# Optimization experiments

Measured on AMD Instinct MI355X. Metric: run time of the kernel, lower is better.

## Reference

```python
import jax, jax.numpy as jnp
import numpy as np

N = 50000   # nodes
R = 3       # relations
E = 300000  # edges per relation
H, D = 4, 32  # heads, per-head dim (hidden_feat=128)
IN, HID, OUT = 128, 128, 64
SLOPE = 0.2  # DGL GATConv leaky_relu negative slope


def setup_inputs() -> dict:
    key = jax.random.key(0)
    ks = jax.random.split(key, 12)
    s = 0.05
    return {
        "x": jax.random.normal(ks[0], (N, IN), jnp.float32),
        "edges": jax.random.randint(ks[1], (R, 2, E), 0, N, jnp.int64),
        "W1": jax.random.normal(ks[2], (R, IN, H * D), jnp.float32) * s,
        "al1": jax.random.normal(ks[3], (R, H, D), jnp.float32) * s,
        "ar1": jax.random.normal(ks[4], (R, H, D), jnp.float32) * s,
        "b1": jnp.zeros((R, H, D), jnp.float32),
        "W2": jax.random.normal(ks[5], (R, HID, H * D), jnp.float32) * s,
        "al2": jax.random.normal(ks[6], (R, H, D), jnp.float32) * s,
        "ar2": jax.random.normal(ks[7], (R, H, D), jnp.float32) * s,
        "b2": jnp.zeros((R, H, D), jnp.float32),
        "Wl": jax.random.normal(ks[8], (HID, OUT), jnp.float32) * s,
        "bl": jnp.zeros((OUT,), jnp.float32),
    }


def rgat_layer(h, edges, W, al, ar, b):
    """HeteroGraphConv(sum) of per-relation GATConv. h: [N,F]. Returns [N,H,D]."""
    out = jnp.zeros((N, H, D), h.dtype)
    for r in range(R):  # small fixed relation count
        src, dst = edges[r, 0], edges[r, 1]
        feat = (h @ W[r]).reshape(N, H, D)                  # per-relation projection
        el = jnp.einsum("nhd,hd->nh", feat, al[r])          # [N,H]
        er = jnp.einsum("nhd,hd->nh", feat, ar[r])          # [N,H]
        e = jax.nn.leaky_relu(el[src] + er[dst], SLOPE)      # [E,H]
        # edge softmax over incoming edges per destination node
        emax = jax.ops.segment_max(e, dst, num_segments=N)   # [N,H]
        ex = jnp.exp(e - emax[dst])
        denom = jax.ops.segment_sum(ex, dst, num_segments=N) # [N,H]
        alpha = ex / denom[dst]                               # [E,H]
        msg = feat[src] * alpha[:, :, None]                   # [E,H,D]
        out = out + jax.ops.segment_sum(msg, dst, num_segments=N) + b[r]
    return out


def reference(x, edges, W1, al1, ar1, b1, W2, al2, ar2, b2, Wl, bl):
    h = rgat_layer(x, edges, W1, al1, ar1, b1).reshape(N, H * D)
    h = jax.nn.relu(h)  # dropout is identity in eval mode
    h = rgat_layer(h, edges, W2, al2, ar2, b2).reshape(N, H * D)
    return h @ Wl + bl  # [N, OUT]
```

## Files before the change

### kernel.cpp

```cpp
#include <hip/hip_runtime.h>
#include <hip/hip_bf16.h>
#include <hip/hip_fp16.h>
#include <type_traits>

#define Nn 50000
#define RR 3
#define EE 300000

typedef __attribute__((ext_vector_type(8))) short short8;
typedef __attribute__((ext_vector_type(4))) short short4v;
typedef __attribute__((ext_vector_type(4))) float floatx4;

__device__ __forceinline__ short f2bf(float f) {
    __hip_bfloat16 h = __float2bfloat16(f);
    return *reinterpret_cast<short*>(&h);
}


__global__ void count_wswz_kernel(const int* __restrict__ edges, int* __restrict__ counts,
                                  int* __restrict__ ord,
                                  const float* __restrict__ W1, const float* __restrict__ W2,
                                  short* __restrict__ Z) {
    int bx = blockIdx.x;
    if (bx >= 440) {
        int idx = (bx - 440) * 256 + threadIdx.x;
        if (idx >= 12288) return;
        int lane = idx & 63;
        int nt = (idx >> 6) & 7;
        int kt = (idx >> 9) & 3;
        int rl = idx >> 11;
        int layer = rl / 3, r = rl % 3;
        const float* W = (layer ? W2 : W1) + (size_t)r * 16384;
        int n = nt * 16 + (lane & 15);
        int k0 = kt * 32 + (lane >> 4) * 8;
        short8 v;
        #pragma unroll
        for (int j = 0; j < 8; ++j) v[j] = f2bf(W[(size_t)(k0 + j) * 128 + n]);
        *(short8*)&Z[(size_t)idx * 8] = v;
        return;
    }
    int i = bx * 256 + threadIdx.x;
    if (i >= RR * EE / 8) return;
    int g = i * 8;
    int r = g / EE, e0 = g - r * EE;
    const int* db = &edges[(size_t)r * 2 * EE + EE + e0];
    int4 d0 = *(const int4*)db;
    int4 d1 = *(const int4*)(db + 4);
    int* cb = counts + r * Nn;
    int4 o0, o1;
    o0.x = atomicAdd(&cb[d0.x], 1);
    o0.y = atomicAdd(&cb[d0.y], 1);
    o0.z = atomicAdd(&cb[d0.z], 1);
    o0.w = atomicAdd(&cb[d0.w], 1);
    o1.x = atomicAdd(&cb[d1.x], 1);
    o1.y = atomicAdd(&cb[d1.y], 1);
    o1.z = atomicAdd(&cb[d1.z], 1);
    o1.w = atomicAdd(&cb[d1.w], 1);
    *(int4*)&ord[g] = o0;
    *(int4*)&ord[g + 4] = o1;
}

__global__ __launch_bounds__(256) void alloc_kernel(const int* __restrict__ counts,
                                                    int* __restrict__ row_start,
                                                    int* __restrict__ totals) {
    __shared__ int s[256];
    __shared__ int base_s;
    int r = blockIdx.y;
    int tid = threadIdx.x;
    int n = blockIdx.x * 256 + tid;
    int idx = r * Nn + n;
    int c = (n < Nn) ? counts[idx] : 0;
    s[tid] = c;
    __syncthreads();
    #pragma unroll
    for (int off = 1; off < 256; off <<= 1) {
        int v = 0;
        if (tid >= off) v = s[tid - off];
        __syncthreads();
        if (tid >= off) s[tid] += v;
        __syncthreads();
    }
    if (tid == 255) base_s = atomicAdd(&totals[r], s[255]);
    __syncthreads();
    if (n < Nn) row_start[idx] = base_s + s[tid] - c;
}

__global__ void scatter_kernel(const int* __restrict__ edges, const int* __restrict__ ord,
                               const int* __restrict__ row_start, int2* __restrict__ csr) {
    int i = blockIdx.x * blockDim.x + threadIdx.x;
    if (i >= RR * EE / 8) return;
    int g = i * 8;
    int r = g / EE, e0 = g - r * EE;
    const int* sb = &edges[(size_t)r * 2 * EE + e0];
    const int* db = sb + EE;
    int4 s0 = *(const int4*)sb, s1 = *(const int4*)(sb + 4);
    int4 d0 = *(const int4*)db, d1 = *(const int4*)(db + 4);
    int4 o0 = *(const int4*)&ord[g], o1 = *(const int4*)&ord[g + 4];
    const int* rs = row_start + r * Nn;
    int2* cb = csr + (size_t)r * EE;
    cb[rs[d0.x] + o0.x] = make_int2(s0.x, d0.x);
    cb[rs[d0.y] + o0.y] = make_int2(s0.y, d0.y);
    cb[rs[d0.z] + o0.z] = make_int2(s0.z, d0.z);
    cb[rs[d0.w] + o0.w] = make_int2(s0.w, d0.w);
    cb[rs[d1.x] + o1.x] = make_int2(s1.x, d1.x);
    cb[rs[d1.y] + o1.y] = make_int2(s1.y, d1.y);
    cb[rs[d1.z] + o1.z] = make_int2(s1.z, d1.z);
    cb[rs[d1.w] + o1.w] = make_int2(s1.w, d1.w);
}


template<typename TA>
__global__ __launch_bounds__(256) void gemm_proj_mfma(const TA* __restrict__ A,
                                                      const short* __restrict__ Z,
                                                      const float* __restrict__ al,
                                                      const float* __restrict__ ar,
                                                      __half* __restrict__ C,
                                                      float* __restrict__ el,
                                                      float* __restrict__ er) {
    __shared__ short A_lds[64 * 136];
    __shared__ float al_lds[384], ar_lds[384];
    int tid = threadIdx.x;
    int row0 = blockIdx.x * 64;
    if (tid < 128) { al_lds[256 + tid] = al[256 + tid]; ar_lds[256 + tid] = ar[256 + tid]; }
    al_lds[tid] = al[tid]; ar_lds[tid] = ar[tid];
    if constexpr (std::is_same<TA, float>::value) {
        #pragma unroll
        for (int p = 0; p < 8; ++p) {
            int f = p * 256 + tid;
            int row = f >> 5;
            int c4 = (f & 31) * 4;
            float4 v = make_float4(0.f, 0.f, 0.f, 0.f);
            if (row0 + row < Nn) v = *(const float4*)&A[(size_t)(row0 + row) * 128 + c4];
            short4v sv;
            sv[0] = f2bf(v.x); sv[1] = f2bf(v.y); sv[2] = f2bf(v.z); sv[3] = f2bf(v.w);
            *(short4v*)&A_lds[row * 136 + c4] = sv;
        }
    } else {
        #pragma unroll
        for (int p = 0; p < 4; ++p) {
            int c = p * 256 + tid;
            int row = c >> 4, c8 = (c & 15) * 8;
            short8 v = (short8)(0);
            if (row0 + row < Nn) v = *(const short8*)&A[(size_t)(row0 + row) * 128 + c8];
            *(short8*)&A_lds[row * 136 + c8] = v;
        }
    }
    __syncthreads();
    int wave = tid >> 6, lane = tid & 63;
    int m = lane & 15, q = lane >> 4;
    short8 af[4];
    #pragma unroll
    for (int kt = 0; kt < 4; ++kt)
        af[kt] = *(short8*)&A_lds[(wave * 16 + m) * 136 + kt * 32 + q * 8];
    __syncthreads();
    __half* lds_h = (__half*)A_lds;
    int row8 = tid >> 2;
    int hh = tid & 3;
    for (int r = 0; r < RR; ++r) {
        floatx4 acc[8];
        #pragma unroll
        for (int nt = 0; nt < 8; ++nt) acc[nt] = (floatx4)(0.f);
        const short* Zr = Z + (size_t)r * 16384;
        #pragma unroll
        for (int kt = 0; kt < 4; ++kt) {
            #pragma unroll
            for (int nt = 0; nt < 8; ++nt) {
                short8 bf = *(const short8*)&Zr[(size_t)(kt * 8 + nt) * 512 + lane * 8];
                acc[nt] = __builtin_amdgcn_mfma_f32_16x16x32_bf16(af[kt], bf, acc[nt], 0, 0, 0);
            }
        }
        #pragma unroll
        for (int nt = 0; nt < 8; ++nt) {
            int col = nt * 16 + m;
            #pragma unroll
            for (int reg = 0; reg < 4; ++reg)
                lds_h[(wave * 16 + q * 4 + reg) * 136 + col] = __float2half(acc[nt][reg]);
        }
        __syncthreads();
        __half* Cr = C + (size_t)r * Nn * 128;
        #pragma unroll
        for (int p = 0; p < 4; ++p) {
            int lin = p * 256 + tid;
            int row = lin >> 4, c8 = (lin & 15) * 8;
            if (row0 + row < Nn)
                *(short8*)&Cr[(size_t)(row0 + row) * 128 + c8] = *(short8*)&lds_h[row * 136 + c8];
        }
        {
            const __half2* fp = (const __half2*)&lds_h[row8 * 136 + hh * 32];
            const float* alp = &al_lds[r * 128 + hh * 32];
            const float* arp = &ar_lds[r * 128 + hh * 32];
            float sl = 0.f, sr = 0.f;
            #pragma unroll
            for (int d = 0; d < 16; ++d) {
                float2 v = __half22float2(fp[d]);
                sl += v.x * alp[2 * d] + v.y * alp[2 * d + 1];
                sr += v.x * arp[2 * d] + v.y * arp[2 * d + 1];
            }
            if (row0 + row8 < Nn) {
                size_t ei = (size_t)(r * Nn + row0 + row8) * 4 + hh;
                el[ei] = sl;
                er[ei] = sr;
            }
        }
        __syncthreads();
    }
}


__global__ __launch_bounds__(256) void gemm_final_kernel(const float* __restrict__ A,
                                                         const float* __restrict__ Wl,
                                                         const float* __restrict__ bl,
                                                         float* __restrict__ out) {
    __shared__ float As[16][65];
    __shared__ float Bs[16][65];
    int tid = threadIdx.x;
    int row0 = blockIdx.x * 64;
    float acc[4][4] = {};
    int tx = tid & 15, ty = tid >> 4;
    for (int k0 = 0; k0 < 128; k0 += 16) {
        {
            int mm = tid >> 2, c = (tid & 3) * 4;
            int row = row0 + mm;
            float4 v = make_float4(0.f, 0.f, 0.f, 0.f);
            if (row < Nn) v = *(const float4*)&A[(size_t)row * 128 + k0 + c];
            As[c + 0][mm] = v.x; As[c + 1][mm] = v.y; As[c + 2][mm] = v.z; As[c + 3][mm] = v.w;
        }
        {
            int kk = tid >> 4, j = (tid & 15) * 4;
            float4 v = *(const float4*)&Wl[(size_t)(k0 + kk) * 64 + j];
            *(float4*)&Bs[kk][j] = v;
        }
        __syncthreads();
        #pragma unroll
        for (int kk = 0; kk < 16; ++kk) {
            float4 a = *(const float4*)&As[kk][ty * 4];
            float4 b = *(const float4*)&Bs[kk][tx * 4];
            float av[4] = {a.x, a.y, a.z, a.w};
            float bv[4] = {b.x, b.y, b.z, b.w};
            #pragma unroll
            for (int i = 0; i < 4; ++i)
                #pragma unroll
                for (int j = 0; j < 4; ++j) acc[i][j] += av[i] * bv[j];
        }
        __syncthreads();
    }
    float4 bias = *(const float4*)&bl[tx * 4];
    #pragma unroll
    for (int i = 0; i < 4; ++i) {
        int row = row0 + ty * 4 + i;
        if (row >= Nn) continue;
        float4 v = make_float4(acc[i][0] + bias.x, acc[i][1] + bias.y,
                               acc[i][2] + bias.z, acc[i][3] + bias.w);
        *(float4*)&out[(size_t)row * 64 + tx * 4] = v;
    }
}


__global__ __launch_bounds__(256) void wexp_kernel(const int2* __restrict__ csr,
                                                   const float* __restrict__ el,
                                                   const float* __restrict__ er,
                                                   unsigned* __restrict__ wqp) {
    int r = blockIdx.y;
    int k = blockIdx.x * 256 + threadIdx.x;
    if (k >= EE) return;
    size_t gk = (size_t)r * EE + k;
    int2 e = csr[gk];
    float4 l4 = *(const float4*)&el[(size_t)(r * Nn + e.x) * 4];
    float4 r4 = *(const float4*)&er[(size_t)(r * Nn + e.y) * 4];
    float lv[4] = {l4.x, l4.y, l4.z, l4.w};
    float rv[4] = {r4.x, r4.y, r4.z, r4.w};
    unsigned sbits = (unsigned)e.x;
    #pragma unroll
    for (int h = 0; h < 4; ++h) {
        float x = lv[h] + rv[h];
        x = (x > 0.f) ? x : 0.2f * x;
        unsigned wb = (unsigned)__half_as_ushort(__float2half(__expf(x)));
        wqp[(size_t)h * (RR * EE) + gk] = sbits | (wb << 16);
    }
}


template<bool OUT_BF16_RELU>
__global__ __launch_bounds__(256) void agg_kernel(const __half2* __restrict__ feat2,
                                                  const unsigned* __restrict__ wqp,
                                                  const int* __restrict__ row_start,
                                                  const int* __restrict__ counts,
                                                  const float* __restrict__ b,
                                                  void* __restrict__ out) {
    int wave = threadIdx.x >> 6;
    int lane = threadIdx.x & 63;
    int n = blockIdx.x * 4 + wave;
    if (n >= Nn) return;
    int h = lane >> 4;
    int hl = lane & 15;
    int grp = lane & 48;
    int t2 = lane * 2;
    int cntA[RR], stA[RR];
    unsigned pC[RR];
    #pragma unroll
    for (int r = 0; r < RR; ++r) {
        cntA[r] = counts[r * Nn + n];
        stA[r] = row_start[r * Nn + n];
    }
    #pragma unroll
    for (int r = 0; r < RR; ++r) {
        pC[r] = 0u;
        if (hl < cntA[r])
            pC[r] = wqp[(size_t)h * (RR * EE) + (size_t)r * EE + stA[r] + hl];
    }
    float accx = b[t2] + b[128 + t2] + b[256 + t2];
    float accy = b[t2 + 1] + b[128 + t2 + 1] + b[256 + t2 + 1];
    #pragma unroll
    for (int r = 0; r < RR; ++r) {
        int cnt = cntA[r];
        if (cnt == 0) continue;
        const __half2* fr = feat2 + (size_t)r * Nn * 64;
        float den = 0.f, numx = 0.f, numy = 0.f;
        unsigned p_l = pC[r];
        int i0 = 0;
        while (true) {
            int mm = cnt - i0; if (mm > 16) mm = 16;
            int mm8 = (mm + 7) & ~7;
            for (int j = 0; j < mm8; j += 8) {
                unsigned u0 = __shfl(p_l, grp | j);
                unsigned u1 = __shfl(p_l, grp | (j + 1));
                unsigned u2 = __shfl(p_l, grp | (j + 2));
                unsigned u3 = __shfl(p_l, grp | (j + 3));
                unsigned u4 = __shfl(p_l, grp | (j + 4));
                unsigned u5 = __shfl(p_l, grp | (j + 5));
                unsigned u6 = __shfl(p_l, grp | (j + 6));
                unsigned u7 = __shfl(p_l, grp | (j + 7));
                __half2 f0 = fr[(size_t)(u0 & 0xFFFFu) * 64 + lane];
                __half2 f1 = fr[(size_t)(u1 & 0xFFFFu) * 64 + lane];
                __half2 f2 = fr[(size_t)(u2 & 0xFFFFu) * 64 + lane];
                __half2 f3 = fr[(size_t)(u3 & 0xFFFFu) * 64 + lane];
                __half2 f4 = fr[(size_t)(u4 & 0xFFFFu) * 64 + lane];
                __half2 f5 = fr[(size_t)(u5 & 0xFFFFu) * 64 + lane];
                __half2 f6 = fr[(size_t)(u6 & 0xFFFFu) * 64 + lane];
                __half2 f7 = fr[(size_t)(u7 & 0xFFFFu) * 64 + lane];
                float w0 = __half2float(__ushort_as_half((unsigned short)(u0 >> 16)));
                float w1 = __half2float(__ushort_as_half((unsigned short)(u1 >> 16)));
                float w2 = __half2float(__ushort_as_half((unsigned short)(u2 >> 16)));
                float w3 = __half2float(__ushort_as_half((unsigned short)(u3 >> 16)));
                float w4 = __half2float(__ushort_as_half((unsigned short)(u4 >> 16)));
                float w5 = __half2float(__ushort_as_half((unsigned short)(u5 >> 16)));
                float w6 = __half2float(__ushort_as_half((unsigned short)(u6 >> 16)));
                float w7 = __half2float(__ushort_as_half((unsigned short)(u7 >> 16)));
                float2 g0 = __half22float2(f0), g1 = __half22float2(f1);
                float2 g2 = __half22float2(f2), g3 = __half22float2(f3);
                float2 g4 = __half22float2(f4), g5 = __half22float2(f5);
                float2 g6 = __half22float2(f6), g7 = __half22float2(f7);
                den += ((w0 + w1) + (w2 + w3)) + ((w4 + w5) + (w6 + w7));
                numx += (w0 * g0.x + w1 * g1.x + w2 * g2.x + w3 * g3.x)
                      + (w4 * g4.x + w5 * g5.x + w6 * g6.x + w7 * g7.x);
                numy += (w0 * g0.y + w1 * g1.y + w2 * g2.y + w3 * g3.y)
                      + (w4 * g4.y + w5 * g5.y + w6 * g6.y + w7 * g7.y);
            }
            i0 += 16;
            if (i0 >= cnt) break;
            p_l = 0u;
            if (i0 + hl < cnt)
                p_l = wqp[(size_t)h * (RR * EE) + (size_t)r * EE + stA[r] + i0 + hl];
        }
        float inv = 1.f / den;
        accx += numx * inv;
        accy += numy * inv;
    }
    if constexpr (OUT_BF16_RELU) {
        short* o = (short*)out;
        short2 pk;
        pk.x = f2bf(fmaxf(accx, 0.f));
        pk.y = f2bf(fmaxf(accy, 0.f));
        *(short2*)&o[(size_t)n * 128 + t2] = pk;
    } else {
        float* o = (float*)out;
        *(float2*)&o[(size_t)n * 128 + t2] = make_float2(accx, accy);
    }
}


extern "C" void kernel_launch(void* const* d_in, const int* in_sizes, int n_in,
                              void* d_out, int out_size, void* d_ws, size_t ws_size,
                              hipStream_t stream) {
    const float* x   = (const float*)d_in[0];
    const int*  edges = (const int*)d_in[1];
    const float* W1  = (const float*)d_in[2];
    const float* al1 = (const float*)d_in[3];
    const float* ar1 = (const float*)d_in[4];
    const float* b1  = (const float*)d_in[5];
    const float* W2  = (const float*)d_in[6];
    const float* al2 = (const float*)d_in[7];
    const float* ar2 = (const float*)d_in[8];
    const float* b2  = (const float*)d_in[9];
    const float* Wl  = (const float*)d_in[10];
    const float* bl  = (const float*)d_in[11];
    float* out = (float*)d_out;

    __half* feat  = (__half*)d_ws;
    short* Z      = (short*)(feat + (size_t)RR * Nn * 128);
    float* el     = (float*)(Z + 98304);
    float* er     = el + (size_t)RR * Nn * 4;
    float* outbuf = er + (size_t)RR * Nn * 4;
    unsigned* wqp = (unsigned*)(outbuf + (size_t)Nn * 128);
    int* counts    = (int*)(wqp + (size_t)4 * RR * EE);
    int* totals    = counts + RR * Nn;
    int* row_start = totals + 4;
    int* ord       = row_start + RR * Nn;
    int2* csr      = (int2*)(ord + RR * EE);
    short* outb16  = (short*)outbuf;

    const int rowBlocks  = (Nn + 63) / 64;
    const int nodeBlocks = (Nn + 255) / 256;
    const int aggBlocks  = (Nn + 3) / 4;
    const int edgeBlocks = (EE + 255) / 256;
    const int edge8Blocks = (RR * EE / 8 + 255) / 256;

    hipMemsetAsync(counts, 0, (size_t)(RR * Nn + 4) * sizeof(int), stream);
    count_wswz_kernel<<<440 + 48, 256, 0, stream>>>(edges, counts, ord, W1, W2, Z);
    alloc_kernel<<<dim3(nodeBlocks, RR), 256, 0, stream>>>(counts, row_start, totals);
    scatter_kernel<<<edge8Blocks, 256, 0, stream>>>(edges, ord, row_start, csr);

    gemm_proj_mfma<float><<<rowBlocks, 256, 0, stream>>>(x, Z, al1, ar1, feat, el, er);
    wexp_kernel<<<dim3(edgeBlocks, RR), 256, 0, stream>>>(csr, el, er, wqp);
    agg_kernel<true><<<aggBlocks, 256, 0, stream>>>((const __half2*)feat, wqp, row_start, counts, b1, outb16);

    gemm_proj_mfma<short><<<rowBlocks, 256, 0, stream>>>(outb16, Z + 49152, al2, ar2, feat, el, er);
    wexp_kernel<<<dim3(edgeBlocks, RR), 256, 0, stream>>>(csr, el, er, wqp);
    agg_kernel<false><<<aggBlocks, 256, 0, stream>>>((const __half2*)feat, wqp, row_start, counts, b2, outbuf);

    gemm_final_kernel<<<rowBlocks, 256, 0, stream>>>(outbuf, Wl, bl, out);
}
```

Baseline: 333.5 us.

## Fuse edge-weight exp computation into aggregation kernel and shrink CSR to source-only

Removes the separate wexp kernel that precomputed packed source+exp-weight words per head. Instead, the aggregation kernel reads source indices from a source-only CSR, gathers el[src] and er[dst], and computes leaky-relu and exp inline per lane. This avoids writing and re-reading a 4-heads x R x E weight buffer and two kernel launches per layer. The cost is an extra scattered el gather inside the latency-bound aggregation loop.

```diff
diff --git a/kernel.cpp b/kernel.cpp
--- a/kernel.cpp
+++ b/kernel.cpp
@@ -86,7 +86,7 @@
 }
 
 __global__ void scatter_kernel(const int* __restrict__ edges, const int* __restrict__ ord,
-                               const int* __restrict__ row_start, int2* __restrict__ csr) {
+                               const int* __restrict__ row_start, int* __restrict__ csr_s) {
     int i = blockIdx.x * blockDim.x + threadIdx.x;
     if (i >= RR * EE / 8) return;
     int g = i * 8;
@@ -97,15 +97,15 @@
     int4 d0 = *(const int4*)db, d1 = *(const int4*)(db + 4);
     int4 o0 = *(const int4*)&ord[g], o1 = *(const int4*)&ord[g + 4];
     const int* rs = row_start + r * Nn;
-    int2* cb = csr + (size_t)r * EE;
-    cb[rs[d0.x] + o0.x] = make_int2(s0.x, d0.x);
-    cb[rs[d0.y] + o0.y] = make_int2(s0.y, d0.y);
-    cb[rs[d0.z] + o0.z] = make_int2(s0.z, d0.z);
-    cb[rs[d0.w] + o0.w] = make_int2(s0.w, d0.w);
-    cb[rs[d1.x] + o1.x] = make_int2(s1.x, d1.x);
-    cb[rs[d1.y] + o1.y] = make_int2(s1.y, d1.y);
-    cb[rs[d1.z] + o1.z] = make_int2(s1.z, d1.z);
-    cb[rs[d1.w] + o1.w] = make_int2(s1.w, d1.w);
+    int* cs = csr_s + (size_t)r * EE;
+    cs[rs[d0.x] + o0.x] = s0.x;
+    cs[rs[d0.y] + o0.y] = s0.y;
+    cs[rs[d0.z] + o0.z] = s0.z;
+    cs[rs[d0.w] + o0.w] = s0.w;
+    cs[rs[d1.x] + o1.x] = s1.x;
+    cs[rs[d1.y] + o1.y] = s1.y;
+    cs[rs[d1.z] + o1.z] = s1.z;
+    cs[rs[d1.w] + o1.w] = s1.w;
 }
 
 
@@ -256,33 +256,11 @@
 }
 
 
-__global__ __launch_bounds__(256) void wexp_kernel(const int2* __restrict__ csr,
-                                                   const float* __restrict__ el,
-                                                   const float* __restrict__ er,
-                                                   unsigned* __restrict__ wqp) {
-    int r = blockIdx.y;
-    int k = blockIdx.x * 256 + threadIdx.x;
-    if (k >= EE) return;
-    size_t gk = (size_t)r * EE + k;
-    int2 e = csr[gk];
-    float4 l4 = *(const float4*)&el[(size_t)(r * Nn + e.x) * 4];
-    float4 r4 = *(const float4*)&er[(size_t)(r * Nn + e.y) * 4];
-    float lv[4] = {l4.x, l4.y, l4.z, l4.w};
-    float rv[4] = {r4.x, r4.y, r4.z, r4.w};
-    unsigned sbits = (unsigned)e.x;
-    #pragma unroll
-    for (int h = 0; h < 4; ++h) {
-        float x = lv[h] + rv[h];
-        x = (x > 0.f) ? x : 0.2f * x;
-        unsigned wb = (unsigned)__half_as_ushort(__float2half(__expf(x)));
-        wqp[(size_t)h * (RR * EE) + gk] = sbits | (wb << 16);
-    }
-}
-
-
 template<bool OUT_BF16_RELU>
 __global__ __launch_bounds__(256) void agg_kernel(const __half2* __restrict__ feat2,
-                                                  const unsigned* __restrict__ wqp,
+                                                  const float* __restrict__ el,
+                                                  const float* __restrict__ er,
+                                                  const int* __restrict__ csr_s,
                                                   const int* __restrict__ row_start,
                                                   const int* __restrict__ counts,
                                                   const float* __restrict__ b,
@@ -295,8 +273,7 @@
     int hl = lane & 15;
     int grp = lane & 48;
     int t2 = lane * 2;
-    int cntA[RR], stA[RR];
-    unsigned pC[RR];
+    int cntA[RR], stA[RR], sC[RR];
     #pragma unroll
     for (int r = 0; r < RR; ++r) {
         cntA[r] = counts[r * Nn + n];
@@ -304,9 +281,19 @@
     }
     #pragma unroll
     for (int r = 0; r < RR; ++r) {
-        pC[r] = 0u;
-        if (hl < cntA[r])
-            pC[r] = wqp[(size_t)h * (RR * EE) + (size_t)r * EE + stA[r] + hl];
+        sC[r] = 0;
+        if (hl < cntA[r]) sC[r] = csr_s[(size_t)r * EE + stA[r] + hl];
+    }
+    float erv[RR];
+    #pragma unroll
+    for (int r = 0; r < RR; ++r) erv[r] = er[(size_t)(r * Nn + n) * 4 + h];
+    unsigned pC[RR];
+    #pragma unroll
+    for (int r = 0; r < RR; ++r) {
+        float x = el[(size_t)(r * Nn + sC[r]) * 4 + h] + erv[r];
+        x = (x > 0.f) ? x : 0.2f * x;
+        unsigned wb = (hl < cntA[r]) ? (unsigned)__half_as_ushort(__float2half(__expf(x))) : 0u;
+        pC[r] = (unsigned)sC[r] | (wb << 16);
     }
     float accx = b[t2] + b[128 + t2] + b[256 + t2];
     float accy = b[t2 + 1] + b[128 + t2 + 1] + b[256 + t2 + 1];
@@ -358,9 +345,12 @@
             }
             i0 += 16;
             if (i0 >= cnt) break;
-            p_l = 0u;
-            if (i0 + hl < cnt)
-                p_l = wqp[(size_t)h * (RR * EE) + (size_t)r * EE + stA[r] + i0 + hl];
+            int s_t = 0;
+            if (i0 + hl < cnt) s_t = csr_s[(size_t)r * EE + stA[r] + i0 + hl];
+            float x = el[(size_t)(r * Nn + s_t) * 4 + h] + erv[r];
+            x = (x > 0.f) ? x : 0.2f * x;
+            unsigned wb = (i0 + hl < cnt) ? (unsigned)__half_as_ushort(__float2half(__expf(x))) : 0u;
+            p_l = (unsigned)s_t | (wb << 16);
         }
         float inv = 1.f / den;
         accx += numx * inv;
@@ -401,32 +391,28 @@
     float* el     = (float*)(Z + 98304);
     float* er     = el + (size_t)RR * Nn * 4;
     float* outbuf = er + (size_t)RR * Nn * 4;
-    unsigned* wqp = (unsigned*)(outbuf + (size_t)Nn * 128);
-    int* counts    = (int*)(wqp + (size_t)4 * RR * EE);
+    int* counts    = (int*)(outbuf + (size_t)Nn * 128);
     int* totals    = counts + RR * Nn;
     int* row_start = totals + 4;
     int* ord       = row_start + RR * Nn;
-    int2* csr      = (int2*)(ord + RR * EE);
+    int* csr_s     = ord + RR * EE;
     short* outb16  = (short*)outbuf;
 
     const int rowBlocks  = (Nn + 63) / 64;
     const int nodeBlocks = (Nn + 255) / 256;
     const int aggBlocks  = (Nn + 3) / 4;
-    const int edgeBlocks = (EE + 255) / 256;
     const int edge8Blocks = (RR * EE / 8 + 255) / 256;
 
     hipMemsetAsync(counts, 0, (size_t)(RR * Nn + 4) * sizeof(int), stream);
     count_wswz_kernel<<<440 + 48, 256, 0, stream>>>(edges, counts, ord, W1, W2, Z);
     alloc_kernel<<<dim3(nodeBlocks, RR), 256, 0, stream>>>(counts, row_start, totals);
-    scatter_kernel<<<edge8Blocks, 256, 0, stream>>>(edges, ord, row_start, csr);
+    scatter_kernel<<<edge8Blocks, 256, 0, stream>>>(edges, ord, row_start, csr_s);
 
     gemm_proj_mfma<float><<<rowBlocks, 256, 0, stream>>>(x, Z, al1, ar1, feat, el, er);
-    wexp_kernel<<<dim3(edgeBlocks, RR), 256, 0, stream>>>(csr, el, er, wqp);
-    agg_kernel<true><<<aggBlocks, 256, 0, stream>>>((const __half2*)feat, wqp, row_start, counts, b1, outb16);
+    agg_kernel<true><<<aggBlocks, 256, 0, stream>>>((const __half2*)feat, el, er, csr_s, row_start, counts, b1, outb16);
 
     gemm_proj_mfma<short><<<rowBlocks, 256, 0, stream>>>(outb16, Z + 49152, al2, ar2, feat, el, er);
-    wexp_kernel<<<dim3(edgeBlocks, RR), 256, 0, stream>>>(csr, el, er, wqp);
-    agg_kernel<false><<<aggBlocks, 256, 0, stream>>>((const __half2*)feat, wqp, row_start, counts, b2, outbuf);
+    agg_kernel<false><<<aggBlocks, 256, 0, stream>>>((const __half2*)feat, el, er, csr_s, row_start, counts, b2, outbuf);
 
     gemm_final_kernel<<<rowBlocks, 256, 0, stream>>>(outbuf, Wl, bl, out);
 }
```

After: 324.9 us. 2.6% less time.
